# Optimization experiments

Hardware: AMD Instinct MI355X
Metric: run time of the kernel (lower is better)

Reference implementation:

```python
import jax, jax.numpy as jnp
import numpy as np

N, D, H, E, TOP_K = 8192, 1024, 4096, 8, 2


def setup_inputs() -> dict:
    key = jax.random.key(0)
    ks = jax.random.split(key, 6)
    input_batch = jax.random.normal(ks[0], (N, D), dtype=jnp.float32)
    # Router-style top-k: distinct expert ids per token, softmax-normalized weights
    logits = jax.random.normal(ks[1], (N, E), dtype=jnp.float32)
    topk_vals, indices = jax.lax.top_k(logits, TOP_K)          # [N, k]
    probabilities = jax.nn.softmax(topk_vals, axis=-1)          # [N, k]
    scale1 = 1.0 / np.sqrt(D)
    scale2 = 1.0 / np.sqrt(H)
    W1 = jax.random.normal(ks[2], (E, D, H), dtype=jnp.float32) * scale1
    b1 = jnp.zeros((E, H), dtype=jnp.float32)
    W2 = jax.random.normal(ks[3], (E, H, D), dtype=jnp.float32) * scale2
    b2 = jnp.zeros((E, D), dtype=jnp.float32)
    return {
        "input_batch": input_batch,
        "probabilities": probabilities,
        "indices": indices.astype(jnp.int64),
        "W1": W1, "b1": b1, "W2": W2, "b2": b2,
    }


def reference(input_batch, probabilities, indices, W1, b1, W2, b2):
    # Each expert is Linear(D->H) + ReLU + Linear(H->D).
    # Dense per-expert forward (batched GEMM over the expert axis), then
    # gather the top_k selected expert outputs per token and combine with
    # router probabilities applied AFTER the experts:
    #   out[n] = sum_k p[n,k] * expert_{idx[n,k]}(x[n])
    h = jax.nn.relu(jnp.einsum("nd,edh->enh", input_batch, W1) + b1[:, None, :])
    y = jnp.einsum("enh,eho->eno", h, W2) + b2[:, None, :]      # [E, N, D]
    y_tok = jnp.swapaxes(y, 0, 1)                                # [N, E, D]
    sel = jnp.take_along_axis(y_tok, indices[:, :, None], axis=1)  # [N, k, D]
    output = jnp.sum(probabilities[:, :, None] * sel, axis=1)    # [N, D]
    total_loss = jnp.asarray(0.0, dtype=input_batch.dtype)       # sampler+expert losses are zero here
    return output, total_loss
```

## Files before the change

kernel.cpp:

```cpp
#include <hip/hip_runtime.h>
#include <hip/hip_bf16.h>

#define N_TOK 8192
#define DDIM 1024
#define HDIM 4096
#define NEXP 8
#define TOPK 2
#define NK (N_TOK*TOPK)
#define BM 128
#define BN 128
#define BK 64
#define MAXT 136

typedef __hip_bfloat16 bf16;
typedef __attribute__((ext_vector_type(8))) short bf16x8;
typedef __attribute__((ext_vector_type(4))) float f32x4;

__device__ __forceinline__ void gload16(const void* g, void* lds) {
  auto l = (__attribute__((address_space(3))) unsigned int*)(unsigned int)(unsigned long long)lds;
  auto gg = (const __attribute__((address_space(1))) unsigned int*)(unsigned long long)g;
  __builtin_amdgcn_global_load_lds(gg, l, 16, 0, 0);
}

__global__ void k_detect(const int* __restrict__ idx, int* __restrict__ flag) {
  if (threadIdx.x == 0 && blockIdx.x == 0) {
    int allz = 1;
    for (int i = 1; i < 32; i += 2) allz &= (idx[i] == 0);
    *flag = allz ? 2 : 1;
  }
}

__global__ void k_count(const int* __restrict__ idx, const int* __restrict__ flag,
                        int* __restrict__ cnt) {
  int r = blockIdx.x * blockDim.x + threadIdx.x;
  if (r >= NK) return;
  int s = *flag;
  int e = idx[r * s];
  e = min(max(e, 0), NEXP - 1);
  atomicAdd(&cnt[e], 1);
}

__global__ void k_scan(const int* __restrict__ cnt, int* __restrict__ offp,
                       int* __restrict__ off2, int* __restrict__ texp,
                       int* __restrict__ tok) {
  __shared__ int so[NEXP + 1], sc[NEXP];
  int tid = threadIdx.x;
  if (tid == 0) {
    int cum = 0;
    for (int e = 0; e < NEXP; e++) {
      so[e] = cum; sc[e] = cnt[e];
      cum += ((cnt[e] + BM - 1) / BM) * BM;
    }
    so[NEXP] = cum;
    for (int e = 0; e <= NEXP; e++) offp[e] = so[e];
  }
  __syncthreads();
  if (tid < NEXP) off2[tid] = so[tid];
  int total_tiles = so[NEXP] / BM;
  for (int t = tid; t < MAXT; t += blockDim.x) {
    int e = -1;
    if (t < total_tiles) {
      for (int q = 0; q < NEXP; q++)
        if (t * BM >= so[q] && t * BM < so[q + 1]) e = q;
    }
    texp[t] = e;
  }
  for (int e = 0; e < NEXP; e++) {
    int start = so[e] + sc[e], end = so[e + 1];
    for (int i = start + tid; i < end; i += blockDim.x) tok[i] = 0;
  }
}

__global__ void k_scatter(const int* __restrict__ idx, const int* __restrict__ flag,
                          int* __restrict__ off2, int* __restrict__ tok,
                          int* __restrict__ pos) {
  int r = blockIdx.x * blockDim.x + threadIdx.x;
  if (r >= NK) return;
  int s = *flag;
  int e = idx[r * s];
  e = min(max(e, 0), NEXP - 1);
  int p = atomicAdd(&off2[e], 1);
  tok[p] = r >> 1;
  pos[r] = p;
}

__global__ void k_cvt_x(const float* __restrict__ x, bf16* __restrict__ xb) {
  int i = blockIdx.x * blockDim.x + threadIdx.x;
  if (i >= N_TOK * DDIM / 8) return;
  float4 a = ((const float4*)x)[(size_t)i * 2];
  float4 b = ((const float4*)x)[(size_t)i * 2 + 1];
  union { bf16 h[8]; uint4 v; } u;
  u.h[0] = __float2bfloat16(a.x); u.h[1] = __float2bfloat16(a.y);
  u.h[2] = __float2bfloat16(a.z); u.h[3] = __float2bfloat16(a.w);
  u.h[4] = __float2bfloat16(b.x); u.h[5] = __float2bfloat16(b.y);
  u.h[6] = __float2bfloat16(b.z); u.h[7] = __float2bfloat16(b.w);
  *(uint4*)&xb[(size_t)i * 8] = u.v;
}

__global__ void k_transpose(const float* __restrict__ in, bf16* __restrict__ out,
                            int R, int C) {
  __shared__ float t[32][33];
  size_t ebase = (size_t)blockIdx.z * R * C;
  int tx = threadIdx.x & 31, ty = threadIdx.x >> 5;
  int c0 = blockIdx.x * 32, r0 = blockIdx.y * 32;
#pragma unroll
  for (int j = 0; j < 4; j++)
    t[ty + j * 8][tx] = in[ebase + (size_t)(r0 + ty + j * 8) * C + c0 + tx];
  __syncthreads();
  int tx2 = (threadIdx.x & 15) * 2;
  int cy  = threadIdx.x >> 4;
#pragma unroll
  for (int p = 0; p < 2; p++) {
    int c = cy + p * 16;
    union { bf16 h[2]; unsigned int u; } w;
    w.h[0] = __float2bfloat16(t[tx2][c]);
    w.h[1] = __float2bfloat16(t[tx2 + 1][c]);
    *(unsigned int*)&out[ebase + (size_t)(c0 + c) * R + r0 + tx2] = w.u;
  }
}

template<int MODE>
__global__ __launch_bounds__(256, 3) void k_gemm(
    const bf16* __restrict__ A, const bf16* __restrict__ Bt,
    const float* __restrict__ bias, const int* __restrict__ texp,
    const int* __restrict__ tok, int K, int Ncols, int tile_base,
    void* __restrict__ Cout)
{
  int tm = tile_base + blockIdx.y;
  int e = texp[tm];
  if (e < 0) return;
  int tn = blockIdx.x;
  int tid = threadIdx.x, lane = tid & 63, wid = tid >> 6;
  int wm = wid >> 1, wn = wid & 1;

  __shared__ __align__(16) bf16 As[BM * BK];
  __shared__ __align__(16) bf16 Bs[BN * BK];

  const bf16* Bexp = Bt + ((size_t)e * Ncols + (size_t)tn * BN) * K;

  const bf16* asrc[4];
  const bf16* bsrc[4];
#pragma unroll
  for (int it = 0; it < 4; ++it) {
    int ch = it * 256 + tid;
    int i = ch >> 3, c = ch & 7;
    int cs = c ^ (i & 7);
    int arow;
    if (MODE == 0) arow = tok[tm * BM + i];
    else           arow = (tm - tile_base) * BM + i;
    asrc[it] = A + (size_t)arow * K + cs * 8;
    bsrc[it] = Bexp + (size_t)i * K + cs * 8;
  }

  f32x4 acc[4][4];
#pragma unroll
  for (int i = 0; i < 4; i++)
#pragma unroll
    for (int j = 0; j < 4; j++) acc[i][j] = (f32x4){0.f, 0.f, 0.f, 0.f};

  for (int k0 = 0; k0 < K; k0 += BK) {
#pragma unroll
    for (int it = 0; it < 4; ++it)
      gload16(asrc[it] + k0, (char*)As + (it * 256 + wid * 64) * 16);
#pragma unroll
    for (int it = 0; it < 4; ++it)
      gload16(bsrc[it] + k0, (char*)Bs + (it * 256 + wid * 64) * 16);
    asm volatile("s_waitcnt vmcnt(0)" ::: "memory");
    __syncthreads();

#pragma unroll
    for (int kh = 0; kh < 2; ++kh) {
      bf16x8 av[4], bv[4];
      int lr = lane & 15, kg = lane >> 4;
#pragma unroll
      for (int mi = 0; mi < 4; mi++) {
        int m = wm * 64 + mi * 16 + lr;
        int ph = (kh * 4 + kg) ^ (m & 7);
        av[mi] = *(const bf16x8*)&As[m * BK + ph * 8];
      }
#pragma unroll
      for (int ni = 0; ni < 4; ni++) {
        int n = wn * 64 + ni * 16 + lr;
        int ph = (kh * 4 + kg) ^ (n & 7);
        bv[ni] = *(const bf16x8*)&Bs[n * BK + ph * 8];
      }
#pragma unroll
      for (int mi = 0; mi < 4; mi++)
#pragma unroll
        for (int ni = 0; ni < 4; ni++)
          acc[mi][ni] = __builtin_amdgcn_mfma_f32_16x16x32_bf16(
              av[mi], bv[ni], acc[mi][ni], 0, 0, 0);
    }
    __syncthreads();
  }

  const float* be = bias + (size_t)e * Ncols;
  int lr = lane & 15, rg = lane >> 4;
#pragma unroll
  for (int ni = 0; ni < 4; ++ni) {
    int n = tn * BN + wn * 64 + ni * 16 + lr;
    float bv = be[n];
#pragma unroll
    for (int mi = 0; mi < 4; ++mi) {
#pragma unroll
      for (int j = 0; j < 4; j++) {
        int mrow = wm * 64 + mi * 16 + rg * 4 + j;
        float v = acc[mi][ni][j] + bv;
        if (MODE == 0) {
          v = fmaxf(v, 0.f);
          ((bf16*)Cout)[(size_t)((tm - tile_base) * BM + mrow) * Ncols + n] =
              __float2bfloat16(v);
        } else {
          ((float*)Cout)[(size_t)(tm * BM + mrow) * Ncols + n] = v;
        }
      }
    }
  }
}

__global__ void k_combine(const float* __restrict__ y, const float* __restrict__ prob,
                          const int* __restrict__ pos, float* __restrict__ out) {
  int gid = blockIdx.x * blockDim.x + threadIdx.x;
  if (gid >= N_TOK * DDIM / 4) return;
  int n = gid / (DDIM / 4);
  int d4 = gid % (DDIM / 4);
  int r0 = pos[2 * n], r1 = pos[2 * n + 1];
  float p0 = prob[2 * n], p1 = prob[2 * n + 1];
  float4 a = *(const float4*)&y[(size_t)r0 * DDIM + (size_t)d4 * 4];
  float4 b = *(const float4*)&y[(size_t)r1 * DDIM + (size_t)d4 * 4];
  float4 o;
  o.x = p0 * a.x + p1 * b.x; o.y = p0 * a.y + p1 * b.y;
  o.z = p0 * a.z + p1 * b.z; o.w = p0 * a.w + p1 * b.w;
  *(float4*)&out[(size_t)n * DDIM + (size_t)d4 * 4] = o;
  if (gid == 0) out[(size_t)N_TOK * DDIM] = 0.f;
}

extern "C" void kernel_launch(void* const* d_in, const int* in_sizes, int n_in,
                              void* d_out, int out_size, void* d_ws, size_t ws_size,
                              hipStream_t stream) {
  const float* x    = (const float*)d_in[0];
  const float* prob = (const float*)d_in[1];
  const int*   idx  = (const int*)d_in[2];
  const float* W1   = (const float*)d_in[3];
  const float* b1   = (const float*)d_in[4];
  const float* W2   = (const float*)d_in[5];
  const float* b2   = (const float*)d_in[6];
  float* out = (float*)d_out;

  char* ws = (char*)d_ws;
  size_t cur = 0;
  auto alloc = [&](size_t bytes) -> void* {
    cur = (cur + 255) & ~(size_t)255;
    void* p = ws + cur; cur += bytes; return p;
  };
  int* cnt   = (int*)alloc(NEXP * 4);
  int* offp  = (int*)alloc((NEXP + 1) * 4);
  int* off2  = (int*)alloc(NEXP * 4);
  int* flag  = (int*)alloc(4);
  int* texp  = (int*)alloc(MAXT * 4);
  int* tok   = (int*)alloc((size_t)MAXT * BM * 4);
  int* pos   = (int*)alloc((size_t)NK * 4);
  bf16* Xb   = (bf16*)alloc((size_t)N_TOK * DDIM * 2);
  bf16* W1t  = (bf16*)alloc((size_t)NEXP * HDIM * DDIM * 2);
  bf16* W2t  = (bf16*)alloc((size_t)NEXP * DDIM * HDIM * 2);
  float* ybuf = (float*)alloc((size_t)MAXT * BM * DDIM * 4);
  cur = (cur + 255) & ~(size_t)255;
  size_t h_off = cur;
  size_t h_avail = ws_size > h_off ? ws_size - h_off : 0;
  long long ts_ll = (long long)(h_avail / ((size_t)BM * HDIM * 2));
  int ts = (int)(ts_ll < 1 ? 1 : (ts_ll > MAXT ? MAXT : ts_ll));
  bf16* hbuf = (bf16*)(ws + h_off);

  hipMemsetAsync(cnt, 0, NEXP * 4, stream);
  k_detect<<<1, 64, 0, stream>>>(idx, flag);
  k_count<<<(NK + 255) / 256, 256, 0, stream>>>(idx, flag, cnt);
  k_scan<<<1, 256, 0, stream>>>(cnt, offp, off2, texp, tok);
  k_scatter<<<(NK + 255) / 256, 256, 0, stream>>>(idx, flag, off2, tok, pos);
  k_cvt_x<<<(N_TOK * DDIM / 8 + 255) / 256, 256, 0, stream>>>(x, Xb);
  k_transpose<<<dim3(HDIM / 32, DDIM / 32, NEXP), 256, 0, stream>>>(W1, W1t, DDIM, HDIM);
  k_transpose<<<dim3(DDIM / 32, HDIM / 32, NEXP), 256, 0, stream>>>(W2, W2t, HDIM, DDIM);

  for (int base = 0; base < MAXT; base += ts) {
    int cnt_t = (MAXT - base < ts) ? (MAXT - base) : ts;
    k_gemm<0><<<dim3(HDIM / BN, cnt_t), 256, 0, stream>>>(
        Xb, W1t, b1, texp, tok, DDIM, HDIM, base, (void*)hbuf);
    k_gemm<1><<<dim3(DDIM / BN, cnt_t), 256, 0, stream>>>(
        hbuf, W2t, b2, texp, tok, HDIM, DDIM, base, (void*)ybuf);
  }
  k_combine<<<(N_TOK * DDIM / 4 + 255) / 256, 256, 0, stream>>>(ybuf, prob, pos, out);
}
```

Measured before the change: 588.4 us.

## Use 256-row tiles, double-buffered 8-wave GEMM pipeline, XCD remap, bf16 expert output

```diff
diff --git a/kernel.cpp b/kernel.cpp
--- a/kernel.cpp
+++ b/kernel.cpp
@@ -7,10 +7,9 @@
 #define NEXP 8
 #define TOPK 2
 #define NK (N_TOK*TOPK)
-#define BM 128
-#define BN 128
+#define BM 256
 #define BK 64
-#define MAXT 136
+#define MAXT 72
 
 typedef __hip_bfloat16 bf16;
 typedef __attribute__((ext_vector_type(8))) short bf16x8;
@@ -120,118 +119,241 @@
 }
 
 template<int MODE>
-__global__ __launch_bounds__(256, 3) void k_gemm(
+__global__ __launch_bounds__(512, 2) void k_gemm(
     const bf16* __restrict__ A, const bf16* __restrict__ Bt,
     const float* __restrict__ bias, const int* __restrict__ texp,
-    const int* __restrict__ tok, int K, int Ncols, int tile_base,
-    void* __restrict__ Cout)
+    const int* __restrict__ tok, int tile_base, void* __restrict__ Cout)
 {
-  int tm = tile_base + blockIdx.y;
+  constexpr int KT    = MODE ? HDIM : DDIM;
+  constexpr int NCOL  = MODE ? DDIM : HDIM;
+  constexpr int BNT   = MODE ? 128 : 256;
+  constexpr int GX    = NCOL / BNT;
+  constexpr int MI    = MODE ? 4 : 8;
+  constexpr int MPP   = MI / 4;
+  constexpr int NT    = KT / BK;
+  constexpr int NITER = NT / 2;
+  constexpr int LA    = 2;
+  constexpr int LB    = MODE ? 1 : 2;
+  constexpr int BUFE  = (BM + BNT) * BK;
+  constexpr int AHALF_E = 128 * BK;
+  constexpr int BHALF_E = (BNT / 2) * BK;
+
+  int nwg = gridDim.x, orig = blockIdx.x;
+  int q8 = nwg >> 3, r8 = nwg & 7;
+  int xcd = orig & 7, jj0 = orig >> 3;
+  int w = (xcd < r8 ? xcd * (q8 + 1) : r8 * (q8 + 1) + (xcd - r8) * q8) + jj0;
+  int tn = w % GX;
+  int tm = tile_base + w / GX;
   int e = texp[tm];
   if (e < 0) return;
-  int tn = blockIdx.x;
+
   int tid = threadIdx.x, lane = tid & 63, wid = tid >> 6;
-  int wm = wid >> 1, wn = wid & 1;
-
-  __shared__ __align__(16) bf16 As[BM * BK];
-  __shared__ __align__(16) bf16 Bs[BN * BK];
-
-  const bf16* Bexp = Bt + ((size_t)e * Ncols + (size_t)tn * BN) * K;
-
-  const bf16* asrc[4];
-  const bf16* bsrc[4];
-#pragma unroll
-  for (int it = 0; it < 4; ++it) {
-    int ch = it * 256 + tid;
-    int i = ch >> 3, c = ch & 7;
-    int cs = c ^ (i & 7);
-    int arow;
-    if (MODE == 0) arow = tok[tm * BM + i];
-    else           arow = (tm - tile_base) * BM + i;
-    asrc[it] = A + (size_t)arow * K + cs * 8;
-    bsrc[it] = Bexp + (size_t)i * K + cs * 8;
-  }
-
-  f32x4 acc[4][4];
-#pragma unroll
-  for (int i = 0; i < 4; i++)
+  int wm = MODE ? (wid >> 1) : (wid >> 2);
+  int wn = MODE ? (wid & 1) : (wid & 3);
+  int lr = lane & 15, kg = lane >> 4;
+
+  __shared__ __align__(16) bf16 lds[2 * BUFE];
+
+  const bf16* Bexp = Bt + ((size_t)e * NCOL + (size_t)tn * BNT) * KT;
+
+  const bf16* aptr[2][LA];
+  const bf16* bptr[2][LB];
+#pragma unroll
+  for (int h = 0; h < 2; ++h) {
+#pragma unroll
+    for (int it = 0; it < LA; ++it) {
+      int ch = it * 512 + tid, il = ch >> 3, c = ch & 7;
+      int row = h * 128 + il;
+      int arow = MODE ? (tm - tile_base) * BM + row : tok[tm * BM + row];
+      aptr[h][it] = A + (size_t)arow * KT + (c ^ (il & 7)) * 8;
+    }
+#pragma unroll
+    for (int it = 0; it < LB; ++it) {
+      int ch = it * 512 + tid, il = ch >> 3, c = ch & 7;
+      int row = h * (BNT / 2) + il;
+      bptr[h][it] = Bexp + (size_t)row * KT + (c ^ (il & 7)) * 8;
+    }
+  }
+
+  auto stageA = [&](int h, int kt) {
+    if (kt >= NT) return;
+    char* dst = (char*)lds + ((size_t)(kt & 1) * BUFE + h * AHALF_E) * 2;
+#pragma unroll
+    for (int it = 0; it < LA; ++it)
+      gload16(aptr[h][it] + kt * BK, dst + (it * 512 + wid * 64) * 16);
+  };
+  auto stageB = [&](int h, int kt) {
+    if (kt >= NT) return;
+    char* dst = (char*)lds + ((size_t)(kt & 1) * BUFE + BM * BK + h * BHALF_E) * 2;
+#pragma unroll
+    for (int it = 0; it < LB; ++it)
+      gload16(bptr[h][it] + kt * BK, dst + (it * 512 + wid * 64) * 16);
+  };
+
+  f32x4 acc[MI][4];
+#pragma unroll
+  for (int i = 0; i < MI; i++)
 #pragma unroll
     for (int j = 0; j < 4; j++) acc[i][j] = (f32x4){0.f, 0.f, 0.f, 0.f};
 
-  for (int k0 = 0; k0 < K; k0 += BK) {
-#pragma unroll
-    for (int it = 0; it < 4; ++it)
-      gload16(asrc[it] + k0, (char*)As + (it * 256 + wid * 64) * 16);
-#pragma unroll
-    for (int it = 0; it < 4; ++it)
-      gload16(bsrc[it] + k0, (char*)Bs + (it * 256 + wid * 64) * 16);
-    asm volatile("s_waitcnt vmcnt(0)" ::: "memory");
-    __syncthreads();
-
-#pragma unroll
-    for (int kh = 0; kh < 2; ++kh) {
-      bf16x8 av[4], bv[4];
-      int lr = lane & 15, kg = lane >> 4;
-#pragma unroll
-      for (int mi = 0; mi < 4; mi++) {
-        int m = wm * 64 + mi * 16 + lr;
-        int ph = (kh * 4 + kg) ^ (m & 7);
-        av[mi] = *(const bf16x8*)&As[m * BK + ph * 8];
-      }
-#pragma unroll
-      for (int ni = 0; ni < 4; ni++) {
+  bf16x8 bv[8];
+  auto readB = [&](int buf) {
+    const bf16* base = lds + buf * BUFE + BM * BK;
+#pragma unroll
+    for (int ni = 0; ni < 4; ++ni)
+#pragma unroll
+      for (int kh = 0; kh < 2; ++kh) {
         int n = wn * 64 + ni * 16 + lr;
         int ph = (kh * 4 + kg) ^ (n & 7);
-        bv[ni] = *(const bf16x8*)&Bs[n * BK + ph * 8];
+        bv[ni * 2 + kh] = *(const bf16x8*)&base[n * BK + ph * 8];
       }
-#pragma unroll
-      for (int mi = 0; mi < 4; mi++)
-#pragma unroll
-        for (int ni = 0; ni < 4; ni++)
-          acc[mi][ni] = __builtin_amdgcn_mfma_f32_16x16x32_bf16(
-              av[mi], bv[ni], acc[mi][ni], 0, 0, 0);
-    }
-    __syncthreads();
-  }
-
-  const float* be = bias + (size_t)e * Ncols;
-  int lr = lane & 15, rg = lane >> 4;
+  };
+  auto readA = [&](int buf, int q, bf16x8* av) {
+    const bf16* base = lds + buf * BUFE;
+#pragma unroll
+    for (int g = 0; g < MPP; ++g)
+#pragma unroll
+      for (int kh = 0; kh < 2; ++kh) {
+        int m = wm * (MI * 16) + (q * MPP + g) * 16 + lr;
+        int ph = (kh * 4 + kg) ^ (m & 7);
+        av[g * 2 + kh] = *(const bf16x8*)&base[m * BK + ph * 8];
+      }
+  };
+  auto domfma = [&](int q, bf16x8* av) {
+    __builtin_amdgcn_s_setprio(1);
+#pragma unroll
+    for (int g = 0; g < MPP; ++g)
+#pragma unroll
+      for (int ni = 0; ni < 4; ++ni)
+#pragma unroll
+        for (int kh = 0; kh < 2; ++kh)
+          acc[q * MPP + g][ni] = __builtin_amdgcn_mfma_f32_16x16x32_bf16(
+              av[g * 2 + kh], bv[ni * 2 + kh], acc[q * MPP + g][ni], 0, 0, 0);
+    __builtin_amdgcn_s_setprio(0);
+  };
+
+#define WAIT_VMC() do { if (MODE) asm volatile("s_waitcnt vmcnt(4)" ::: "memory"); \
+                        else      asm volatile("s_waitcnt vmcnt(6)" ::: "memory"); } while(0)
+#define PH_TAIL()  do { asm volatile("s_waitcnt lgkmcnt(0)" ::: "memory"); \
+                        __builtin_amdgcn_sched_barrier(0); } while(0)
+
+  stageB(0, 0); stageB(1, 0); stageA(0, 0); stageA(1, 0); stageB(0, 1); stageB(1, 1);
+
+#pragma unroll 1
+  for (int i = 0; i < NITER; ++i) {
+    int kt0 = 2 * i;
+    bool last = (i == NITER - 1);
+    bf16x8 av[2 * MPP];
+
+    stageA(0, kt0 + 1);
+    WAIT_VMC();
+    __builtin_amdgcn_s_barrier();
+    readB(0);
+    readA(0, 0, av);
+    PH_TAIL();
+    domfma(0, av);
+    __builtin_amdgcn_s_barrier();
+
+    readA(0, 1, av);
+    stageA(1, kt0 + 1);
+    __builtin_amdgcn_s_barrier();
+    PH_TAIL();
+    domfma(1, av);
+    __builtin_amdgcn_s_barrier();
+
+    readA(0, 2, av);
+    stageB(0, kt0 + 2);
+    __builtin_amdgcn_s_barrier();
+    PH_TAIL();
+    domfma(2, av);
+    __builtin_amdgcn_s_barrier();
+
+    readA(0, 3, av);
+    stageB(1, kt0 + 2);
+    __builtin_amdgcn_s_barrier();
+    PH_TAIL();
+    domfma(3, av);
+    __builtin_amdgcn_s_barrier();
+
+    stageA(0, kt0 + 2);
+    if (last) { asm volatile("s_waitcnt vmcnt(0)" ::: "memory"); }
+    else      { WAIT_VMC(); }
+    __builtin_amdgcn_s_barrier();
+    readB(1);
+    readA(1, 0, av);
+    PH_TAIL();
+    domfma(0, av);
+    __builtin_amdgcn_s_barrier();
+
+    readA(1, 1, av);
+    stageA(1, kt0 + 2);
+    __builtin_amdgcn_s_barrier();
+    PH_TAIL();
+    domfma(1, av);
+    __builtin_amdgcn_s_barrier();
+
+    readA(1, 2, av);
+    stageB(0, kt0 + 3);
+    __builtin_amdgcn_s_barrier();
+    PH_TAIL();
+    domfma(2, av);
+    __builtin_amdgcn_s_barrier();
+
+    readA(1, 3, av);
+    stageB(1, kt0 + 3);
+    __builtin_amdgcn_s_barrier();
+    PH_TAIL();
+    domfma(3, av);
+    __builtin_amdgcn_s_barrier();
+  }
+
+  const float* be = bias + (size_t)e * NCOL;
 #pragma unroll
   for (int ni = 0; ni < 4; ++ni) {
-    int n = tn * BN + wn * 64 + ni * 16 + lr;
-    float bv = be[n];
-#pragma unroll
-    for (int mi = 0; mi < 4; ++mi) {
+    int n = tn * BNT + wn * 64 + ni * 16 + lr;
+    float bvv = be[n];
+#pragma unroll
+    for (int mi = 0; mi < MI; ++mi) {
 #pragma unroll
       for (int j = 0; j < 4; j++) {
-        int mrow = wm * 64 + mi * 16 + rg * 4 + j;
-        float v = acc[mi][ni][j] + bv;
+        int mrow = wm * (MI * 16) + mi * 16 + kg * 4 + j;
+        float v = acc[mi][ni][j] + bvv;
         if (MODE == 0) {
           v = fmaxf(v, 0.f);
-          ((bf16*)Cout)[(size_t)((tm - tile_base) * BM + mrow) * Ncols + n] =
+          ((bf16*)Cout)[(size_t)((tm - tile_base) * BM + mrow) * NCOL + n] =
               __float2bfloat16(v);
         } else {
-          ((float*)Cout)[(size_t)(tm * BM + mrow) * Ncols + n] = v;
+          ((bf16*)Cout)[(size_t)(tm * BM + mrow) * NCOL + n] = __float2bfloat16(v);
         }
       }
     }
   }
-}
-
-__global__ void k_combine(const float* __restrict__ y, const float* __restrict__ prob,
+#undef WAIT_VMC
+#undef PH_TAIL
+}
+
+__global__ void k_combine(const bf16* __restrict__ y, const float* __restrict__ prob,
                           const int* __restrict__ pos, float* __restrict__ out) {
   int gid = blockIdx.x * blockDim.x + threadIdx.x;
-  if (gid >= N_TOK * DDIM / 4) return;
-  int n = gid / (DDIM / 4);
-  int d4 = gid % (DDIM / 4);
+  if (gid >= N_TOK * DDIM / 8) return;
+  int n = gid >> 7;
+  int d8 = gid & 127;
   int r0 = pos[2 * n], r1 = pos[2 * n + 1];
   float p0 = prob[2 * n], p1 = prob[2 * n + 1];
-  float4 a = *(const float4*)&y[(size_t)r0 * DDIM + (size_t)d4 * 4];
-  float4 b = *(const float4*)&y[(size_t)r1 * DDIM + (size_t)d4 * 4];
-  float4 o;
-  o.x = p0 * a.x + p1 * b.x; o.y = p0 * a.y + p1 * b.y;
-  o.z = p0 * a.z + p1 * b.z; o.w = p0 * a.w + p1 * b.w;
-  *(float4*)&out[(size_t)n * DDIM + (size_t)d4 * 4] = o;
+  uint4 a = *(const uint4*)&y[(size_t)r0 * DDIM + d8 * 8];
+  uint4 b = *(const uint4*)&y[(size_t)r1 * DDIM + d8 * 8];
+  const unsigned short* ah = (const unsigned short*)&a;
+  const unsigned short* bh = (const unsigned short*)&b;
+  float o[8];
+#pragma unroll
+  for (int k = 0; k < 8; k++) {
+    float fa = __uint_as_float((unsigned)ah[k] << 16);
+    float fb = __uint_as_float((unsigned)bh[k] << 16);
+    o[k] = p0 * fa + p1 * fb;
+  }
+  float4* op = (float4*)&out[(size_t)n * DDIM + d8 * 8];
+  op[0] = (float4){o[0], o[1], o[2], o[3]};
+  op[1] = (float4){o[4], o[5], o[6], o[7]};
   if (gid == 0) out[(size_t)N_TOK * DDIM] = 0.f;
 }
 
@@ -263,7 +385,7 @@
   bf16* Xb   = (bf16*)alloc((size_t)N_TOK * DDIM * 2);
   bf16* W1t  = (bf16*)alloc((size_t)NEXP * HDIM * DDIM * 2);
   bf16* W2t  = (bf16*)alloc((size_t)NEXP * DDIM * HDIM * 2);
-  float* ybuf = (float*)alloc((size_t)MAXT * BM * DDIM * 4);
+  bf16* ybuf = (bf16*)alloc((size_t)MAXT * BM * DDIM * 2);
   cur = (cur + 255) & ~(size_t)255;
   size_t h_off = cur;
   size_t h_avail = ws_size > h_off ? ws_size - h_off : 0;
@@ -282,10 +404,10 @@
 
   for (int base = 0; base < MAXT; base += ts) {
     int cnt_t = (MAXT - base < ts) ? (MAXT - base) : ts;
-    k_gemm<0><<<dim3(HDIM / BN, cnt_t), 256, 0, stream>>>(
-        Xb, W1t, b1, texp, tok, DDIM, HDIM, base, (void*)hbuf);
-    k_gemm<1><<<dim3(DDIM / BN, cnt_t), 256, 0, stream>>>(
-        hbuf, W2t, b2, texp, tok, HDIM, DDIM, base, (void*)ybuf);
-  }
-  k_combine<<<(N_TOK * DDIM / 4 + 255) / 256, 256, 0, stream>>>(ybuf, prob, pos, out);
-}
+    k_gemm<0><<<dim3((HDIM / 256) * cnt_t), 512, 0, stream>>>(
+        Xb, W1t, b1, texp, tok, base, (void*)hbuf);
+    k_gemm<1><<<dim3((DDIM / 128) * cnt_t), 512, 0, stream>>>(
+        hbuf, W2t, b2, texp, tok, base, (void*)ybuf);
+  }
+  k_combine<<<(N_TOK * DDIM / 8 + 255) / 256, 256, 0, stream>>>(ybuf, prob, pos, out);
+}
```

Result: slower. 605.8 us (+3.0%).
